# Performance work log

Measured on AMD Instinct MI355X. Metric: run time of the kernel, lower is better.

Reference implementation:

```python
import jax, jax.numpy as jnp
import numpy as np

N_NODES = 50000
N_EDGES = 800000
IN_F, HID_F, OUT_F = 128, 64, 32
N_GRAPHS = 128


def setup_inputs() -> dict:
    key = jax.random.key(0)
    ks = jax.random.split(key, 8)
    x = jax.random.normal(ks[0], (N_NODES, IN_F), dtype=jnp.float32)
    edge_index = jax.random.randint(ks[1], (2, N_EDGES), 0, N_NODES, dtype=jnp.int64)
    edge_features = jax.random.uniform(ks[2], (N_EDGES,), dtype=jnp.float32)
    batch = jnp.sort(jax.random.randint(ks[3], (N_NODES,), 0, N_GRAPHS, dtype=jnp.int64))
    W = jax.random.normal(ks[4], (IN_F, HID_F), dtype=jnp.float32) / np.sqrt(IN_F)
    b = jax.random.normal(ks[5], (HID_F,), dtype=jnp.float32) * 0.01
    W1 = jax.random.normal(ks[6], (HID_F, OUT_F), dtype=jnp.float32) / np.sqrt(HID_F)
    b1 = jax.random.normal(ks[7], (OUT_F,), dtype=jnp.float32) * 0.01
    return {"x": x, "edge_index": edge_index, "edge_features": edge_features,
            "batch": batch, "num_graphs": N_GRAPHS, "W": W, "b": b, "W1": W1, "b1": b1}


def _gcn_conv(x, edge_index, edge_weight, W, b):
    # Standard GCNConv: add self-loops (weight 1), symmetric normalization,
    # transform-then-aggregate.
    n = x.shape[0]
    loop = jnp.arange(n, dtype=edge_index.dtype)
    src = jnp.concatenate([edge_index[0], loop])
    dst = jnp.concatenate([edge_index[1], loop])
    ew = jnp.concatenate([edge_weight, jnp.ones((n,), edge_weight.dtype)])
    deg = jax.ops.segment_sum(ew, dst, num_segments=n)          # [N]
    dinv = jnp.where(deg > 0, jax.lax.rsqrt(deg), 0.0)
    norm = dinv[src] * ew * dinv[dst]                           # [E+N]
    h = x @ W                                                   # [N, H]
    msg = h[src] * norm[:, None]                                # gather + scale
    out = jax.ops.segment_sum(msg, dst, num_segments=n)         # scatter-add
    return out + b


def reference(x, edge_index, edge_features, batch, num_graphs, W, b, W1, b1):
    h = _gcn_conv(x, edge_index, edge_features, W, b)
    h = jnp.tanh(h)
    # dropout is identity at inference
    node_embeddings = h
    sums = jax.ops.segment_sum(h, batch, num_segments=num_graphs)           # [G, H]
    cnts = jax.ops.segment_sum(jnp.ones((h.shape[0],), h.dtype), batch,
                               num_segments=num_graphs)                      # [G]
    graph_embeddings = sums / jnp.maximum(cnts, 1.0)[:, None]
    graph_embeddings = jnp.tanh(graph_embeddings @ W1 + b1)
    return (graph_embeddings, node_embeddings)
```

## Files before the change

### kernel.cpp

```cpp
#include <hip/hip_runtime.h>
#include <math.h>

#define N_NODES  50000
#define N_EDGES  800000
#define IN_F     128
#define HID_F    64
#define OUT_F    32
#define N_GRAPHS 128
#define SCAN_BLOCKS ((N_NODES + 255) / 256)

__global__ __launch_bounds__(256) void histo_kernel(const int* __restrict__ dst,
                                                    int* __restrict__ cnt,
                                                    int* __restrict__ epos) {
    int e = blockIdx.x * 256 + threadIdx.x;
    if (e < N_EDGES) {
        epos[e] = atomicAdd(&cnt[dst[e]], 1);
    }
}

__global__ __launch_bounds__(256) void scan_partial_kernel(const int* __restrict__ cnt,
                                                           int* __restrict__ partials) {
    __shared__ int red[4];
    int i = blockIdx.x * 256 + threadIdx.x;
    int v = (i < N_NODES) ? cnt[i] : 0;
#pragma unroll
    for (int off = 32; off; off >>= 1) v += __shfl_down(v, off, 64);
    int w = threadIdx.x >> 6;
    if ((threadIdx.x & 63) == 0) red[w] = v;
    __syncthreads();
    if (threadIdx.x == 0) partials[blockIdx.x] = red[0] + red[1] + red[2] + red[3];
}

__global__ __launch_bounds__(256) void scan_top_kernel(const int* __restrict__ partials,
                                                       int* __restrict__ ppref) {
    __shared__ int buf[256];
    int t = threadIdx.x;
    buf[t] = (t < SCAN_BLOCKS) ? partials[t] : 0;
    __syncthreads();
    for (int off = 1; off < 256; off <<= 1) {
        int v = (t >= off) ? buf[t - off] : 0;
        __syncthreads();
        buf[t] += v;
        __syncthreads();
    }
    if (t < SCAN_BLOCKS) ppref[t] = (t > 0) ? buf[t - 1] : 0;
}

__global__ __launch_bounds__(256) void scan_final_kernel(const int* __restrict__ cnt,
                                                         const int* __restrict__ ppref,
                                                         int* __restrict__ offsets) {
    __shared__ int buf[256];
    int t = threadIdx.x;
    int i = blockIdx.x * 256 + t;
    int v = (i < N_NODES) ? cnt[i] : 0;
    buf[t] = v;
    __syncthreads();
    for (int off = 1; off < 256; off <<= 1) {
        int x = (t >= off) ? buf[t - off] : 0;
        __syncthreads();
        buf[t] += x;
        __syncthreads();
    }
    if (i < N_NODES) offsets[i] = ppref[blockIdx.x] + buf[t] - v;
}

__global__ __launch_bounds__(256) void bucket_kernel(const int* __restrict__ src,
                                                     const int* __restrict__ dst,
                                                     const float* __restrict__ ew,
                                                     const int* __restrict__ epos,
                                                     const int* __restrict__ offsets,
                                                     int2* __restrict__ edat) {
    int e = blockIdx.x * 256 + threadIdx.x;
    if (e < N_EDGES) {
        int d   = dst[e];
        int pos = offsets[d] + epos[e];
        edat[pos] = make_int2(src[e], __float_as_int(ew[e]));
    }
}

__global__ __launch_bounds__(256) void degw_kernel(const int* __restrict__ offsets,
                                                   const int* __restrict__ cnt,
                                                   const int2* __restrict__ edat,
                                                   float* __restrict__ dinv) {
    int n = blockIdx.x * 256 + threadIdx.x;
    if (n >= N_NODES) return;
    int beg = offsets[n], end = beg + cnt[n];
    float s = 1.0f;
    for (int j = beg; j < end; ++j) s += __int_as_float(edat[j].y);
    dinv[n] = 1.0f / sqrtf(s);
}

__global__ __launch_bounds__(256) void gemm_kernel(const float* __restrict__ x,
                                                   const float* __restrict__ W,
                                                   const float* __restrict__ dinv,
                                                   float* __restrict__ hs) {
    __shared__ float Ws[IN_F][HID_F];
    int tid = threadIdx.x;
    for (int i = tid * 4; i < IN_F * HID_F; i += 256 * 4) {
        *(float4*)&((float*)Ws)[i] = *(const float4*)&W[i];
    }
    __syncthreads();

    int row = blockIdx.x * 64 + (tid >> 2);
    int c0  = (tid & 3) * 16;
    if (row >= N_NODES) return;

    float acc[16];
#pragma unroll
    for (int j = 0; j < 16; ++j) acc[j] = 0.0f;

    const float* xr = x + (size_t)row * IN_F;
    for (int k = 0; k < IN_F; k += 4) {
        float4 xv = *(const float4*)&xr[k];
#pragma unroll
        for (int j = 0; j < 16; ++j) {
            acc[j] += xv.x * Ws[k + 0][c0 + j];
            acc[j] += xv.y * Ws[k + 1][c0 + j];
            acc[j] += xv.z * Ws[k + 2][c0 + j];
            acc[j] += xv.w * Ws[k + 3][c0 + j];
        }
    }
    float dv = dinv[row];
    float* hr = hs + (size_t)row * HID_F + c0;
#pragma unroll
    for (int j = 0; j < 16; j += 4) {
        *(float4*)&hr[j] = make_float4(acc[j] * dv, acc[j + 1] * dv,
                                       acc[j + 2] * dv, acc[j + 3] * dv);
    }
}

__global__ __launch_bounds__(256) void aggregate_kernel(const float* __restrict__ hs,
                                                        const int* __restrict__ offsets,
                                                        const int* __restrict__ cnt,
                                                        const int2* __restrict__ edat,
                                                        const float* __restrict__ dinv,
                                                        const float* __restrict__ b,
                                                        float* __restrict__ nout) {
    int node = blockIdx.x * 4 + (threadIdx.x >> 6);
    if (node >= N_NODES) return;
    int f   = threadIdx.x & 63;
    int beg = offsets[node];
    int end = beg + cnt[node];

    float acc0 = 0.0f, acc1 = 0.0f;
    int j = beg;
    for (; j + 1 < end; j += 2) {
        int2 e0 = edat[j];
        int2 e1 = edat[j + 1];
        acc0 += hs[(size_t)e0.x * HID_F + f] * __int_as_float(e0.y);
        acc1 += hs[(size_t)e1.x * HID_F + f] * __int_as_float(e1.y);
    }
    if (j < end) {
        int2 e0 = edat[j];
        acc0 += hs[(size_t)e0.x * HID_F + f] * __int_as_float(e0.y);
    }

    float v = dinv[node] * (acc0 + acc1 + hs[(size_t)node * HID_F + f]) + b[f];
    nout[(size_t)node * HID_F + f] = tanhf(v);
}

__global__ void bounds_kernel(const int* __restrict__ batch, int* __restrict__ bounds) {
    int g = threadIdx.x;
    if (g > N_GRAPHS) return;
    int lo = 0, hi = N_NODES;
    while (lo < hi) {
        int m = (lo + hi) >> 1;
        if (batch[m] < g) lo = m + 1; else hi = m;
    }
    bounds[g] = lo;
}

__global__ __launch_bounds__(256) void pool_kernel(const float* __restrict__ ne,
                                                   const int* __restrict__ bounds,
                                                   const float* __restrict__ W1,
                                                   const float* __restrict__ b1,
                                                   float* __restrict__ gout) {
    __shared__ float part[4][HID_F];
    __shared__ float mean_s[HID_F];
    int g  = blockIdx.x;
    int f  = threadIdx.x & 63;
    int w  = threadIdx.x >> 6;
    int lo = bounds[g], hi = bounds[g + 1];

    float s = 0.0f;
    for (int i = lo + w; i < hi; i += 4) s += ne[(size_t)i * HID_F + f];
    part[w][f] = s;
    __syncthreads();

    if (w == 0) {
        float m   = part[0][f] + part[1][f] + part[2][f] + part[3][f];
        float cnt = (float)(hi - lo);
        mean_s[f] = m / fmaxf(cnt, 1.0f);
    }
    __syncthreads();

    int o = threadIdx.x;
    if (o < OUT_F) {
        float acc = b1[o];
        for (int k = 0; k < HID_F; ++k) acc += mean_s[k] * W1[k * OUT_F + o];
        gout[(size_t)g * OUT_F + o] = tanhf(acc);
    }
}

extern "C" void kernel_launch(void* const* d_in, const int* in_sizes, int n_in,
                              void* d_out, int out_size, void* d_ws, size_t ws_size,
                              hipStream_t stream) {
    const float* x   = (const float*)d_in[0];
    const int*   ei  = (const int*)d_in[1];
    const float* ew  = (const float*)d_in[2];
    const int*   bat = (const int*)d_in[3];
    const float* W   = (const float*)d_in[5];
    const float* b   = (const float*)d_in[6];
    const float* W1  = (const float*)d_in[7];
    const float* b1  = (const float*)d_in[8];

    const int* src = ei;
    const int* dst = ei + N_EDGES;

    float* gout = (float*)d_out;
    float* nout = (float*)d_out + (size_t)N_GRAPHS * OUT_F;

    float* ws_f     = (float*)d_ws;
    float* dinv     = ws_f;
    float* hs       = ws_f + 50000;
    int*   cnt      = (int*)(ws_f + 3250000);
    int*   offsets  = (int*)(ws_f + 3300000);
    int*   partials = (int*)(ws_f + 3350000);
    int*   ppref    = (int*)(ws_f + 3350256);
    int*   epos     = (int*)(ws_f + 3350512);
    int2*  edat     = (int2*)(ws_f + 4150512);
    int*   bounds   = (int*)(ws_f + 5750512);

    hipMemsetAsync(cnt, 0, (size_t)N_NODES * sizeof(int), stream);

    histo_kernel<<<(N_EDGES + 255) / 256, 256, 0, stream>>>(dst, cnt, epos);

    scan_partial_kernel<<<SCAN_BLOCKS, 256, 0, stream>>>(cnt, partials);
    scan_top_kernel<<<1, 256, 0, stream>>>(partials, ppref);
    scan_final_kernel<<<SCAN_BLOCKS, 256, 0, stream>>>(cnt, ppref, offsets);

    bucket_kernel<<<(N_EDGES + 255) / 256, 256, 0, stream>>>(src, dst, ew, epos,
                                                             offsets, edat);

    degw_kernel<<<SCAN_BLOCKS, 256, 0, stream>>>(offsets, cnt, edat, dinv);

    gemm_kernel<<<(N_NODES + 63) / 64, 256, 0, stream>>>(x, W, dinv, hs);

    aggregate_kernel<<<(N_NODES + 3) / 4, 256, 0, stream>>>(hs, offsets, cnt, edat,
                                                            dinv, b, nout);

    bounds_kernel<<<1, 256, 0, stream>>>(bat, bounds);
    pool_kernel<<<N_GRAPHS, 256, 0, stream>>>(nout, bounds, W1, b1, gout);
}
```

Baseline: 261.2 us.

## Fuse GEMM with edge histogram, store hidden features in fp16, apply dinv in aggregate

The GEMM no longer scales rows by dinv, so it can run before the degree computation. It now shares one launch with the edge histogram, using disjoint block ranges. The hidden features are stored as fp16, which halves the bytes the random gathers in the aggregate kernel have to read. In exchange, aggregate does an extra dinv[src] load per edge, and fp16 storage loses some precision.

```diff
diff --git a/kernel.cpp b/kernel.cpp
--- a/kernel.cpp
+++ b/kernel.cpp
@@ -1,4 +1,5 @@
 #include <hip/hip_runtime.h>
+#include <hip/hip_fp16.h>
 #include <math.h>
 
 #define N_NODES  50000
@@ -7,14 +8,52 @@
 #define HID_F    64
 #define OUT_F    32
 #define N_GRAPHS 128
-#define SCAN_BLOCKS ((N_NODES + 255) / 256)
-
-__global__ __launch_bounds__(256) void histo_kernel(const int* __restrict__ dst,
-                                                    int* __restrict__ cnt,
-                                                    int* __restrict__ epos) {
-    int e = blockIdx.x * 256 + threadIdx.x;
-    if (e < N_EDGES) {
-        epos[e] = atomicAdd(&cnt[dst[e]], 1);
+#define SCAN_BLOCKS  ((N_NODES + 255) / 256)
+#define GEMM_BLOCKS  ((N_NODES + 63) / 64)
+#define HISTO_BLOCKS ((N_EDGES + 255) / 256)
+
+__global__ __launch_bounds__(256) void fused_gemm_histo(const float* __restrict__ x,
+                                                        const float* __restrict__ W,
+                                                        __half* __restrict__ hs_h,
+                                                        const int* __restrict__ dst,
+                                                        int* __restrict__ cnt,
+                                                        int* __restrict__ epos) {
+    __shared__ float Ws[IN_F][HID_F];
+    if (blockIdx.x >= GEMM_BLOCKS) {
+        int e = (blockIdx.x - GEMM_BLOCKS) * 256 + threadIdx.x;
+        if (e < N_EDGES) epos[e] = atomicAdd(&cnt[dst[e]], 1);
+        return;
+    }
+
+    int tid = threadIdx.x;
+    for (int i = tid * 4; i < IN_F * HID_F; i += 256 * 4) {
+        *(float4*)&((float*)Ws)[i] = *(const float4*)&W[i];
+    }
+    __syncthreads();
+
+    int row = blockIdx.x * 64 + (tid >> 2);
+    int c0  = (tid & 3) * 16;
+    if (row >= N_NODES) return;
+
+    float acc[16];
+#pragma unroll
+    for (int j = 0; j < 16; ++j) acc[j] = 0.0f;
+
+    const float* xr = x + (size_t)row * IN_F;
+    for (int k = 0; k < IN_F; k += 4) {
+        float4 xv = *(const float4*)&xr[k];
+#pragma unroll
+        for (int j = 0; j < 16; ++j) {
+            acc[j] += xv.x * Ws[k + 0][c0 + j];
+            acc[j] += xv.y * Ws[k + 1][c0 + j];
+            acc[j] += xv.z * Ws[k + 2][c0 + j];
+            acc[j] += xv.w * Ws[k + 3][c0 + j];
+        }
+    }
+    __half* hr = hs_h + (size_t)row * HID_F + c0;
+#pragma unroll
+    for (int j = 0; j < 16; j += 2) {
+        *(__half2*)&hr[j] = __floats2half2_rn(acc[j], acc[j + 1]);
     }
 }
 
@@ -90,46 +129,7 @@
     dinv[n] = 1.0f / sqrtf(s);
 }
 
-__global__ __launch_bounds__(256) void gemm_kernel(const float* __restrict__ x,
-                                                   const float* __restrict__ W,
-                                                   const float* __restrict__ dinv,
-                                                   float* __restrict__ hs) {
-    __shared__ float Ws[IN_F][HID_F];
-    int tid = threadIdx.x;
-    for (int i = tid * 4; i < IN_F * HID_F; i += 256 * 4) {
-        *(float4*)&((float*)Ws)[i] = *(const float4*)&W[i];
-    }
-    __syncthreads();
-
-    int row = blockIdx.x * 64 + (tid >> 2);
-    int c0  = (tid & 3) * 16;
-    if (row >= N_NODES) return;
-
-    float acc[16];
-#pragma unroll
-    for (int j = 0; j < 16; ++j) acc[j] = 0.0f;
-
-    const float* xr = x + (size_t)row * IN_F;
-    for (int k = 0; k < IN_F; k += 4) {
-        float4 xv = *(const float4*)&xr[k];
-#pragma unroll
-        for (int j = 0; j < 16; ++j) {
-            acc[j] += xv.x * Ws[k + 0][c0 + j];
-            acc[j] += xv.y * Ws[k + 1][c0 + j];
-            acc[j] += xv.z * Ws[k + 2][c0 + j];
-            acc[j] += xv.w * Ws[k + 3][c0 + j];
-        }
-    }
-    float dv = dinv[row];
-    float* hr = hs + (size_t)row * HID_F + c0;
-#pragma unroll
-    for (int j = 0; j < 16; j += 4) {
-        *(float4*)&hr[j] = make_float4(acc[j] * dv, acc[j + 1] * dv,
-                                       acc[j + 2] * dv, acc[j + 3] * dv);
-    }
-}
-
-__global__ __launch_bounds__(256) void aggregate_kernel(const float* __restrict__ hs,
+__global__ __launch_bounds__(256) void aggregate_kernel(const __half* __restrict__ hs_h,
                                                         const int* __restrict__ offsets,
                                                         const int* __restrict__ cnt,
                                                         const int2* __restrict__ edat,
@@ -147,15 +147,20 @@
     for (; j + 1 < end; j += 2) {
         int2 e0 = edat[j];
         int2 e1 = edat[j + 1];
-        acc0 += hs[(size_t)e0.x * HID_F + f] * __int_as_float(e0.y);
-        acc1 += hs[(size_t)e1.x * HID_F + f] * __int_as_float(e1.y);
+        float w0 = dinv[e0.x] * __int_as_float(e0.y);
+        float w1 = dinv[e1.x] * __int_as_float(e1.y);
+        acc0 += __half2float(hs_h[(size_t)e0.x * HID_F + f]) * w0;
+        acc1 += __half2float(hs_h[(size_t)e1.x * HID_F + f]) * w1;
     }
     if (j < end) {
         int2 e0 = edat[j];
-        acc0 += hs[(size_t)e0.x * HID_F + f] * __int_as_float(e0.y);
-    }
-
-    float v = dinv[node] * (acc0 + acc1 + hs[(size_t)node * HID_F + f]) + b[f];
+        acc0 += __half2float(hs_h[(size_t)e0.x * HID_F + f]) *
+                (dinv[e0.x] * __int_as_float(e0.y));
+    }
+
+    float dn = dinv[node];
+    float self = __half2float(hs_h[(size_t)node * HID_F + f]) * dn;
+    float v = dn * (acc0 + acc1 + self) + b[f];
     nout[(size_t)node * HID_F + f] = tanhf(v);
 }
 
@@ -220,33 +225,32 @@
     float* gout = (float*)d_out;
     float* nout = (float*)d_out + (size_t)N_GRAPHS * OUT_F;
 
-    float* ws_f     = (float*)d_ws;
-    float* dinv     = ws_f;
-    float* hs       = ws_f + 50000;
-    int*   cnt      = (int*)(ws_f + 3250000);
-    int*   offsets  = (int*)(ws_f + 3300000);
-    int*   partials = (int*)(ws_f + 3350000);
-    int*   ppref    = (int*)(ws_f + 3350256);
-    int*   epos     = (int*)(ws_f + 3350512);
-    int2*  edat     = (int2*)(ws_f + 4150512);
-    int*   bounds   = (int*)(ws_f + 5750512);
+    float*  ws_f     = (float*)d_ws;
+    float*  dinv     = ws_f;
+    __half* hs_h     = (__half*)(ws_f + 50000);
+    int*    cnt      = (int*)(ws_f + 1650000);
+    int*    offsets  = (int*)(ws_f + 1700000);
+    int*    partials = (int*)(ws_f + 1750000);
+    int*    ppref    = (int*)(ws_f + 1750256);
+    int*    epos     = (int*)(ws_f + 1750512);
+    int2*   edat     = (int2*)(ws_f + 2550512);
+    int*    bounds   = (int*)(ws_f + 4150512);
 
     hipMemsetAsync(cnt, 0, (size_t)N_NODES * sizeof(int), stream);
 
-    histo_kernel<<<(N_EDGES + 255) / 256, 256, 0, stream>>>(dst, cnt, epos);
+    fused_gemm_histo<<<GEMM_BLOCKS + HISTO_BLOCKS, 256, 0, stream>>>(
+        x, W, hs_h, dst, cnt, epos);
 
     scan_partial_kernel<<<SCAN_BLOCKS, 256, 0, stream>>>(cnt, partials);
     scan_top_kernel<<<1, 256, 0, stream>>>(partials, ppref);
     scan_final_kernel<<<SCAN_BLOCKS, 256, 0, stream>>>(cnt, ppref, offsets);
 
-    bucket_kernel<<<(N_EDGES + 255) / 256, 256, 0, stream>>>(src, dst, ew, epos,
-                                                             offsets, edat);
+    bucket_kernel<<<HISTO_BLOCKS, 256, 0, stream>>>(src, dst, ew, epos,
+                                                    offsets, edat);
 
     degw_kernel<<<SCAN_BLOCKS, 256, 0, stream>>>(offsets, cnt, edat, dinv);
 
-    gemm_kernel<<<(N_NODES + 63) / 64, 256, 0, stream>>>(x, W, dinv, hs);
-
-    aggregate_kernel<<<(N_NODES + 3) / 4, 256, 0, stream>>>(hs, offsets, cnt, edat,
+    aggregate_kernel<<<(N_NODES + 3) / 4, 256, 0, stream>>>(hs_h, offsets, cnt, edat,
                                                             dinv, b, nout);
 
     bounds_kernel<<<1, 256, 0, stream>>>(bat, bounds);
```

Result: faster. 238.8 us (-8.6%).
